# Optimization experiments

Hardware: AMD Instinct MI355X
Metric: run time of the kernel (lower is better)

The kernel has to match this reference:

```python
import jax, jax.numpy as jnp
import numpy as np

N = 50000      # nodes
D = 128        # in_dim
O = 128        # out_dim
MAX_DEG = 32   # degrees uniform in [0, MAX_DEG]


def setup_inputs() -> dict:
    rng = np.random.default_rng(0)
    deg = rng.integers(0, MAX_DEG + 1, size=N)          # includes deg==0 nodes
    dst = np.repeat(np.arange(N), deg)                  # target node per edge (grouped, like the buckets)
    E = dst.shape[0]                                    # ~800000
    src = rng.integers(0, N, size=E)                    # neighbor index per edge (flat neighbor_list)

    key = jax.random.key(0)
    k1, k2, k3, k4 = jax.random.split(key, 4)
    scale = jnp.float32(1.0 / np.sqrt(D))
    return {
        "x":  jax.random.normal(k1, (N, D), jnp.float32),
        "Wg": jax.random.normal(k2, (O, D), jnp.float32) * scale,  # global_lin.weight
        "Wl": jax.random.normal(k3, (O, D), jnp.float32) * scale,  # local_lin.weight
        "Ws": jax.random.normal(k4, (O, D), jnp.float32) * scale,  # self_lin.weight
        "b":  jnp.zeros((O,), jnp.float32),                        # bias param
        "src": jnp.asarray(src, jnp.int32),
        "dst": jnp.asarray(dst, jnp.int32),
        "deg": jnp.asarray(deg, jnp.int32),
    }


def reference(x, Wg, Wl, Ws, b, src, dst, deg):
    n = x.shape[0]
    # global branch: applied to every node
    g_out = x @ Wg.T                                           # [N, O]
    # mean-aggregate neighbor features (gather + segment-sum == the per-bucket view().mean())
    neigh_sum = jax.ops.segment_sum(x[src], dst, num_segments=n)   # [N, D]
    degf = jnp.maximum(deg, 1).astype(x.dtype)[:, None]
    neigh_mean = neigh_sum * (1.0 / degf)                       # [N, D]
    # local + self branches only for deg > 0 (deg==0 bucket keeps just global_out)
    mask = (deg > 0).astype(x.dtype)[:, None]                   # [N, 1]
    out = g_out + mask * (neigh_mean @ Wl.T + x @ Ws.T) + b
    # dropout is identity in eval mode; ELU activation
    return jax.nn.elu(out)
```

## Files before the change

### kernel.cpp

```cpp
#include <hip/hip_runtime.h>
#include <cstdint>
#include <cstddef>

#define GNPB 8
#define MNPB 16
#define GAST 264
#define DFRNG 512
#define VP_BLOCKS 16
#define VPG_BLOCKS 8

typedef __attribute__((ext_vector_type(8))) short bf16x8;
typedef __attribute__((ext_vector_type(4))) float f32x4;

static __device__ __forceinline__ unsigned short f2bf(float f) {
    unsigned int u = __builtin_bit_cast(unsigned int, f);
    u += 0x7fffu + ((u >> 16) & 1u);
    return (unsigned short)(u >> 16);
}
static __device__ __forceinline__ float bfhi(unsigned int u) { return __builtin_bit_cast(float, u & 0xFFFF0000u); }
static __device__ __forceinline__ float bflo(unsigned int u) { return __builtin_bit_cast(float, u << 16); }
static __device__ __forceinline__ void acc8(float* a, const uint4& v, unsigned m) {
    unsigned x0 = v.x & m, x1 = v.y & m, x2 = v.z & m, x3 = v.w & m;
    a[0] += bflo(x0); a[1] += bfhi(x0); a[2] += bflo(x1); a[3] += bfhi(x1);
    a[4] += bflo(x2); a[5] += bfhi(x2); a[6] += bflo(x3); a[7] += bfhi(x3);
}

__global__ __launch_bounds__(256)
void prep(const float* __restrict__ x, const float* __restrict__ Wg,
          const float* __restrict__ Wl, const float* __restrict__ Ws,
          const int* __restrict__ dst,
          unsigned short* __restrict__ Vp, unsigned short* __restrict__ Vpg,
          unsigned short* __restrict__ xb, int* __restrict__ blkoff,
          int total8, int nblk_g, int noffb, int E) {
    const int bx = blockIdx.x, t = threadIdx.x;
    if (bx < VP_BLOCKS) {
        int gid = bx * 256 + t;
        if (gid < 4096) {
            int l = gid & 63, srow = (gid >> 6) & 7, g = gid >> 9;
            int o = g * 16 + (l & 15);
            int k = srow * 32 + (l >> 4) * 8;
            uint4 u;
            if (k < 128) {
                const float* pg = Wg + o * 128 + k;
                const float* ps = Ws + o * 128 + k;
                u.x = (unsigned)f2bf(pg[0]+ps[0]) | ((unsigned)f2bf(pg[1]+ps[1]) << 16);
                u.y = (unsigned)f2bf(pg[2]+ps[2]) | ((unsigned)f2bf(pg[3]+ps[3]) << 16);
                u.z = (unsigned)f2bf(pg[4]+ps[4]) | ((unsigned)f2bf(pg[5]+ps[5]) << 16);
                u.w = (unsigned)f2bf(pg[6]+ps[6]) | ((unsigned)f2bf(pg[7]+ps[7]) << 16);
            } else {
                const float* pl = Wl + o * 128 + (k - 128);
                u.x = (unsigned)f2bf(pl[0]) | ((unsigned)f2bf(pl[1]) << 16);
                u.y = (unsigned)f2bf(pl[2]) | ((unsigned)f2bf(pl[3]) << 16);
                u.z = (unsigned)f2bf(pl[4]) | ((unsigned)f2bf(pl[5]) << 16);
                u.w = (unsigned)f2bf(pl[6]) | ((unsigned)f2bf(pl[7]) << 16);
            }
            ((uint4*)Vp)[gid] = u;
        }
    } else if (bx < VP_BLOCKS + VPG_BLOCKS) {
        int gid = (bx - VP_BLOCKS) * 256 + t;
        if (gid < 2048) {
            int l = gid & 63, s = (gid >> 6) & 3, g = gid >> 8;
            int o = g * 16 + (l & 15);
            int k = s * 32 + (l >> 4) * 8;
            const float* p = Wg + o * 128 + k;
            uint4 u;
            u.x = (unsigned)f2bf(p[0]) | ((unsigned)f2bf(p[1]) << 16);
            u.y = (unsigned)f2bf(p[2]) | ((unsigned)f2bf(p[3]) << 16);
            u.z = (unsigned)f2bf(p[4]) | ((unsigned)f2bf(p[5]) << 16);
            u.w = (unsigned)f2bf(p[6]) | ((unsigned)f2bf(p[7]) << 16);
            ((uint4*)Vpg)[gid] = u;
        }
    } else if (bx < VP_BLOCKS + VPG_BLOCKS + noffb) {
        int b = (bx - VP_BLOCKS - VPG_BLOCKS) * 256 + t;
        if (b < nblk_g) {
            int target = b * GNPB;
            int lo = 0, hi = E;
            while (lo < hi) { int mid = (lo + hi) >> 1; if (dst[mid] < target) lo = mid + 1; else hi = mid; }
            blkoff[b] = lo;
        }
    } else {
        int gid = (bx - VP_BLOCKS - VPG_BLOCKS - noffb) * 256 + t;
        if (gid < total8) {
            const float4* px = (const float4*)x + (size_t)gid * 2;
            float4 a = px[0], bq = px[1];
            uint4 u;
            u.x = (unsigned)f2bf(a.x)  | ((unsigned)f2bf(a.y)  << 16);
            u.y = (unsigned)f2bf(a.z)  | ((unsigned)f2bf(a.w)  << 16);
            u.z = (unsigned)f2bf(bq.x) | ((unsigned)f2bf(bq.y) << 16);
            u.w = (unsigned)f2bf(bq.z) | ((unsigned)f2bf(bq.w) << 16);
            ((uint4*)xb)[gid] = u;
        }
    }
}

__global__ __launch_bounds__(512, 7)
void gather(const unsigned short* __restrict__ xb, const int* __restrict__ src,
            const int* __restrict__ deg, const int* __restrict__ blkoff,
            unsigned short* __restrict__ M, int N) {
    const int t = threadIdx.x, wv = t >> 6, lane = t & 63;
    const int c = lane & 15, p = lane >> 4;
    const int base = blockIdx.x * GNPB;

    int dg8 = 0;
    if (lane < GNPB && base + lane < N) dg8 = deg[base + lane];
    int incl = dg8;
#pragma unroll
    for (int off = 1; off < GNPB; off <<= 1) {
        int v = __shfl_up(incl, off, 64);
        if (lane >= off) incl += v;
    }
    const int d = __shfl(dg8, wv, 64);
    const int s = blkoff[blockIdx.x] + __shfl(incl, wv, 64) - d;
    const int n = base + wv;
    if (n >= N) return;

    int idx = 0;
    if (lane < d) idx = src[s + lane];

    const uint4* x4 = (const uint4*)xb;
    int r0 = __shfl(idx, p, 64),      r1 = __shfl(idx, p + 4, 64);
    int r2 = __shfl(idx, p + 8, 64),  r3 = __shfl(idx, p + 12, 64);
    uint4 v0 = x4[(size_t)r0 * 16 + c], v1 = x4[(size_t)r1 * 16 + c];
    uint4 v2 = x4[(size_t)r2 * 16 + c], v3 = x4[(size_t)r3 * 16 + c];
    uint4 v4, v5, v6, v7;
    const bool two = (d > 16);
    if (two) {
        int e = 16 + p;
        int r4 = __shfl(idx, e, 64),      r5 = __shfl(idx, e + 4, 64);
        int r6 = __shfl(idx, e + 8, 64),  r7 = __shfl(idx, e + 12, 64);
        v4 = x4[(size_t)r4 * 16 + c]; v5 = x4[(size_t)r5 * 16 + c];
        v6 = x4[(size_t)r6 * 16 + c]; v7 = x4[(size_t)r7 * 16 + c];
    }
    float a[8] = {0,0,0,0,0,0,0,0};
    float b[8] = {0,0,0,0,0,0,0,0};
    acc8(a, v0, (p      < d) ? ~0u : 0u);
    acc8(b, v1, (p + 4  < d) ? ~0u : 0u);
    acc8(a, v2, (p + 8  < d) ? ~0u : 0u);
    acc8(b, v3, (p + 12 < d) ? ~0u : 0u);
    if (two) {
        int e = 16 + p;
        acc8(a, v4, (e      < d) ? ~0u : 0u);
        acc8(b, v5, (e + 4  < d) ? ~0u : 0u);
        acc8(a, v6, (e + 8  < d) ? ~0u : 0u);
        acc8(b, v7, (e + 12 < d) ? ~0u : 0u);
    }
#pragma unroll
    for (int i = 0; i < 8; ++i) a[i] += b[i];
#pragma unroll
    for (int i = 0; i < 8; ++i) {
        a[i] += __shfl_xor(a[i], 16, 64);
        a[i] += __shfl_xor(a[i], 32, 64);
    }
    if (p == 0) {
        float inv = (d > 0) ? 1.0f / (float)d : 0.0f;
        uint4 u;
        u.x = (unsigned)f2bf(a[0]*inv) | ((unsigned)f2bf(a[1]*inv) << 16);
        u.y = (unsigned)f2bf(a[2]*inv) | ((unsigned)f2bf(a[3]*inv) << 16);
        u.z = (unsigned)f2bf(a[4]*inv) | ((unsigned)f2bf(a[5]*inv) << 16);
        u.w = (unsigned)f2bf(a[6]*inv) | ((unsigned)f2bf(a[7]*inv) << 16);
        ((uint4*)M)[(size_t)n * 16 + c] = u;
    }
}

__global__ __launch_bounds__(256)
void gemm(const unsigned short* __restrict__ xb, const unsigned short* __restrict__ Mm,
          const int* __restrict__ deg, const unsigned short* __restrict__ Vp,
          const unsigned short* __restrict__ Vpg, const float* __restrict__ bias,
          float* __restrict__ out, int N, int ngemm) {
    __shared__ __align__(16) unsigned short As[MNPB * GAST];
    const int t = threadIdx.x, wv = t >> 6, lane = t & 63;
    const int c = lane & 15, quad = lane >> 4;
    const int g0 = 2 * wv, g1 = 2 * wv + 1;
    const int col0 = g0 * 16 + c, col1 = g1 * 16 + c;
    const float bv0 = bias[col0], bv1 = bias[col1];

    if (blockIdx.x >= ngemm) {
        __shared__ int nds[DFRNG];
        __shared__ int ncnt;
        const int rb = (blockIdx.x - ngemm) * DFRNG;
        if (t == 0) ncnt = 0;
        __syncthreads();
#pragma unroll
        for (int i = 0; i < DFRNG / 256; ++i) {
            int n = rb + i * 256 + t;
            if (n < N && deg[n] == 0) nds[atomicAdd(&ncnt, 1)] = n;
        }
        __syncthreads();
        const int cnt = ncnt;
        if (cnt == 0) return;
        const bf16x8* VB = (const bf16x8*)Vpg;
        for (int base = 0; base < cnt; base += 16) {
            {
                int row = t >> 4, ch = t & 15;
                int i = base + row; if (i > cnt - 1) i = cnt - 1;
                int node = nds[i];
                uint4 val = *(const uint4*)(xb + (size_t)node * 128 + ch * 8);
                *(uint4*)(As + row * GAST + ch * 8) = val;
            }
            bf16x8 b0 = VB[(g0 * 4) * 64 + lane];
            bf16x8 b1 = VB[(g1 * 4) * 64 + lane];
            __syncthreads();
            f32x4 acc0 = (f32x4){0.f,0.f,0.f,0.f};
            f32x4 acc1 = (f32x4){0.f,0.f,0.f,0.f};
#pragma unroll
            for (int s2 = 0; s2 < 4; ++s2) {
                int sn = (s2 + 1) & 3;
                bf16x8 n0 = VB[(g0 * 4 + sn) * 64 + lane];
                bf16x8 n1 = VB[(g1 * 4 + sn) * 64 + lane];
                bf16x8 a0 = *(const bf16x8*)(As + c * GAST + s2 * 32 + quad * 8);
                acc0 = __builtin_amdgcn_mfma_f32_16x16x32_bf16(a0, b0, acc0, 0, 0, 0);
                acc1 = __builtin_amdgcn_mfma_f32_16x16x32_bf16(a0, b1, acc1, 0, 0, 0);
                b0 = n0; b1 = n1;
            }
#pragma unroll
            for (int reg = 0; reg < 4; ++reg) {
                int i = base + quad * 4 + reg;
                if (i < cnt) {
                    int n = nds[i];
                    float v0 = acc0[reg] + bv0;
                    float v1 = acc1[reg] + bv1;
                    out[(size_t)n * 128 + col0] = (v0 > 0.f) ? v0 : __expf(v0) - 1.0f;
                    out[(size_t)n * 128 + col1] = (v1 > 0.f) ? v1 : __expf(v1) - 1.0f;
                }
            }
            __syncthreads();
        }
        return;
    }

    __shared__ unsigned char srowok[MNPB];
    const int base = blockIdx.x * MNPB;
    if (t < MNPB) srowok[t] = (base + t < N && deg[base + t] > 0) ? 1 : 0;
#pragma unroll
    for (int it = 0; it < 2; ++it) {
        int f = it * 256 + t;
        int row = f >> 5, ch = f & 31;
        int grow = base + row; if (grow > N - 1) grow = N - 1;
        const unsigned short* gp = (ch < 16)
            ? xb + (size_t)grow * 128 + ch * 8
            : Mm + (size_t)grow * 128 + (ch - 16) * 8;
        uint4 val = *(const uint4*)gp;
        *(uint4*)(As + row * GAST + ch * 8) = val;
    }
    const bf16x8* VB = (const bf16x8*)Vp;
    bf16x8 b0 = VB[(g0 * 8) * 64 + lane];
    bf16x8 b1 = VB[(g1 * 8) * 64 + lane];
    __syncthreads();

    f32x4 acc0 = (f32x4){0.f, 0.f, 0.f, 0.f};
    f32x4 acc1 = (f32x4){0.f, 0.f, 0.f, 0.f};
#pragma unroll
    for (int s2 = 0; s2 < 8; ++s2) {
        int sn = (s2 + 1) & 7;
        bf16x8 n0 = VB[(g0 * 8 + sn) * 64 + lane];
        bf16x8 n1 = VB[(g1 * 8 + sn) * 64 + lane];
        bf16x8 a0 = *(const bf16x8*)(As + c * GAST + s2 * 32 + quad * 8);
        acc0 = __builtin_amdgcn_mfma_f32_16x16x32_bf16(a0, b0, acc0, 0, 0, 0);
        acc1 = __builtin_amdgcn_mfma_f32_16x16x32_bf16(a0, b1, acc1, 0, 0, 0);
        b0 = n0; b1 = n1;
    }

#pragma unroll
    for (int reg = 0; reg < 4; ++reg) {
        int lrow = quad * 4 + reg;
        int grow = base + lrow;
        if (grow < N && srowok[lrow]) {
            float v0 = acc0[reg] + bv0;
            float v1 = acc1[reg] + bv1;
            out[(size_t)grow * 128 + col0] = (v0 > 0.f) ? v0 : __expf(v0) - 1.0f;
            out[(size_t)grow * 128 + col1] = (v1 > 0.f) ? v1 : __expf(v1) - 1.0f;
        }
    }
}

extern "C" void kernel_launch(void* const* d_in, const int* in_sizes, int n_in,
                              void* d_out, int out_size, void* d_ws, size_t ws_size,
                              hipStream_t stream) {
    const float* x  = (const float*)d_in[0];
    const float* Wg = (const float*)d_in[1];
    const float* Wl = (const float*)d_in[2];
    const float* Ws = (const float*)d_in[3];
    const float* b  = (const float*)d_in[4];
    const int*   src = (const int*)d_in[5];
    const int*   dst = (const int*)d_in[6];
    const int*   deg = (const int*)d_in[7];
    const int E = in_sizes[5];
    const int N = in_sizes[7];
    float* out = (float*)d_out;

    const size_t NB = (size_t)N * 128 * 2;
    unsigned short* Vp     = (unsigned short*)d_ws;
    unsigned short* Vpg    = (unsigned short*)((char*)d_ws + 65536);
    int*            blkoff = (int*)((char*)d_ws + 98304);
    unsigned short* xb     = (unsigned short*)((char*)d_ws + 131072);
    unsigned short* Mm     = (unsigned short*)((char*)d_ws + 131072 + NB);

    const int nblk_g = (N + GNPB - 1) / GNPB;
    const int noffb  = (nblk_g + 255) / 256;
    const int total8 = N * 16;
    const int nconv  = (total8 + 255) / 256;
    const int ngemm  = (N + MNPB - 1) / MNPB;
    const int ndeg   = (N + DFRNG - 1) / DFRNG;

    prep<<<dim3(VP_BLOCKS + VPG_BLOCKS + noffb + nconv), dim3(256), 0, stream>>>(
        x, Wg, Wl, Ws, dst, Vp, Vpg, xb, blkoff, total8, nblk_g, noffb, E);
    gather<<<dim3(nblk_g), dim3(512), 0, stream>>>(xb, src, deg, blkoff, Mm, N);
    gemm<<<dim3(ngemm + ndeg), dim3(256), 0, stream>>>(xb, Mm, deg, Vp, Vpg, b, out, N, ngemm);
}
```

Measured before the change: 137.9 us.

## Fuse neighbor gather-mean into the GEMM kernel via shared memory

Merges the gather kernel and the GEMM kernel into one 512-thread kernel. Each block computes the neighbor means for its 16 nodes, writes them straight into the shared A tile, then runs the MFMA GEMM. Each wave now handles one 16-column output tile instead of two. This removes the global round trip of the bf16 mean matrix and one kernel launch. In exchange it lowers the occupancy bound, and each wave does two gather passes serially before the GEMM.

```diff
diff --git a/kernel.cpp b/kernel.cpp
--- a/kernel.cpp
+++ b/kernel.cpp
@@ -93,86 +93,14 @@
     }
 }
 
-__global__ __launch_bounds__(512, 7)
-void gather(const unsigned short* __restrict__ xb, const int* __restrict__ src,
-            const int* __restrict__ deg, const int* __restrict__ blkoff,
-            unsigned short* __restrict__ M, int N) {
+__global__ __launch_bounds__(512, 5)
+void ggemm(const unsigned short* __restrict__ xb, const int* __restrict__ src,
+           const int* __restrict__ deg, const int* __restrict__ blkoff,
+           const unsigned short* __restrict__ Vp, const unsigned short* __restrict__ Vpg,
+           const float* __restrict__ bias, float* __restrict__ out, int N, int ngemm) {
+    __shared__ __align__(16) unsigned short As[MNPB * GAST];
     const int t = threadIdx.x, wv = t >> 6, lane = t & 63;
     const int c = lane & 15, p = lane >> 4;
-    const int base = blockIdx.x * GNPB;
-
-    int dg8 = 0;
-    if (lane < GNPB && base + lane < N) dg8 = deg[base + lane];
-    int incl = dg8;
-#pragma unroll
-    for (int off = 1; off < GNPB; off <<= 1) {
-        int v = __shfl_up(incl, off, 64);
-        if (lane >= off) incl += v;
-    }
-    const int d = __shfl(dg8, wv, 64);
-    const int s = blkoff[blockIdx.x] + __shfl(incl, wv, 64) - d;
-    const int n = base + wv;
-    if (n >= N) return;
-
-    int idx = 0;
-    if (lane < d) idx = src[s + lane];
-
-    const uint4* x4 = (const uint4*)xb;
-    int r0 = __shfl(idx, p, 64),      r1 = __shfl(idx, p + 4, 64);
-    int r2 = __shfl(idx, p + 8, 64),  r3 = __shfl(idx, p + 12, 64);
-    uint4 v0 = x4[(size_t)r0 * 16 + c], v1 = x4[(size_t)r1 * 16 + c];
-    uint4 v2 = x4[(size_t)r2 * 16 + c], v3 = x4[(size_t)r3 * 16 + c];
-    uint4 v4, v5, v6, v7;
-    const bool two = (d > 16);
-    if (two) {
-        int e = 16 + p;
-        int r4 = __shfl(idx, e, 64),      r5 = __shfl(idx, e + 4, 64);
-        int r6 = __shfl(idx, e + 8, 64),  r7 = __shfl(idx, e + 12, 64);
-        v4 = x4[(size_t)r4 * 16 + c]; v5 = x4[(size_t)r5 * 16 + c];
-        v6 = x4[(size_t)r6 * 16 + c]; v7 = x4[(size_t)r7 * 16 + c];
-    }
-    float a[8] = {0,0,0,0,0,0,0,0};
-    float b[8] = {0,0,0,0,0,0,0,0};
-    acc8(a, v0, (p      < d) ? ~0u : 0u);
-    acc8(b, v1, (p + 4  < d) ? ~0u : 0u);
-    acc8(a, v2, (p + 8  < d) ? ~0u : 0u);
-    acc8(b, v3, (p + 12 < d) ? ~0u : 0u);
-    if (two) {
-        int e = 16 + p;
-        acc8(a, v4, (e      < d) ? ~0u : 0u);
-        acc8(b, v5, (e + 4  < d) ? ~0u : 0u);
-        acc8(a, v6, (e + 8  < d) ? ~0u : 0u);
-        acc8(b, v7, (e + 12 < d) ? ~0u : 0u);
-    }
-#pragma unroll
-    for (int i = 0; i < 8; ++i) a[i] += b[i];
-#pragma unroll
-    for (int i = 0; i < 8; ++i) {
-        a[i] += __shfl_xor(a[i], 16, 64);
-        a[i] += __shfl_xor(a[i], 32, 64);
-    }
-    if (p == 0) {
-        float inv = (d > 0) ? 1.0f / (float)d : 0.0f;
-        uint4 u;
-        u.x = (unsigned)f2bf(a[0]*inv) | ((unsigned)f2bf(a[1]*inv) << 16);
-        u.y = (unsigned)f2bf(a[2]*inv) | ((unsigned)f2bf(a[3]*inv) << 16);
-        u.z = (unsigned)f2bf(a[4]*inv) | ((unsigned)f2bf(a[5]*inv) << 16);
-        u.w = (unsigned)f2bf(a[6]*inv) | ((unsigned)f2bf(a[7]*inv) << 16);
-        ((uint4*)M)[(size_t)n * 16 + c] = u;
-    }
-}
-
-__global__ __launch_bounds__(256)
-void gemm(const unsigned short* __restrict__ xb, const unsigned short* __restrict__ Mm,
-          const int* __restrict__ deg, const unsigned short* __restrict__ Vp,
-          const unsigned short* __restrict__ Vpg, const float* __restrict__ bias,
-          float* __restrict__ out, int N, int ngemm) {
-    __shared__ __align__(16) unsigned short As[MNPB * GAST];
-    const int t = threadIdx.x, wv = t >> 6, lane = t & 63;
-    const int c = lane & 15, quad = lane >> 4;
-    const int g0 = 2 * wv, g1 = 2 * wv + 1;
-    const int col0 = g0 * 16 + c, col1 = g1 * 16 + c;
-    const float bv0 = bias[col0], bv1 = bias[col1];
 
     if (blockIdx.x >= ngemm) {
         __shared__ int nds[DFRNG];
@@ -180,47 +108,42 @@
         const int rb = (blockIdx.x - ngemm) * DFRNG;
         if (t == 0) ncnt = 0;
         __syncthreads();
-#pragma unroll
-        for (int i = 0; i < DFRNG / 256; ++i) {
-            int n = rb + i * 256 + t;
+        {
+            int n = rb + t;
             if (n < N && deg[n] == 0) nds[atomicAdd(&ncnt, 1)] = n;
         }
         __syncthreads();
         const int cnt = ncnt;
         if (cnt == 0) return;
         const bf16x8* VB = (const bf16x8*)Vpg;
+        const int col = wv * 16 + c;
+        const float bv = bias[col];
         for (int base = 0; base < cnt; base += 16) {
-            {
+            if (t < 256) {
                 int row = t >> 4, ch = t & 15;
                 int i = base + row; if (i > cnt - 1) i = cnt - 1;
                 int node = nds[i];
-                uint4 val = *(const uint4*)(xb + (size_t)node * 128 + ch * 8);
-                *(uint4*)(As + row * GAST + ch * 8) = val;
-            }
-            bf16x8 b0 = VB[(g0 * 4) * 64 + lane];
-            bf16x8 b1 = VB[(g1 * 4) * 64 + lane];
+                *(uint4*)(As + row * GAST + ch * 8) =
+                    *(const uint4*)(xb + (size_t)node * 128 + ch * 8);
+            }
+            bf16x8 b0 = VB[(wv * 4) * 64 + lane];
             __syncthreads();
-            f32x4 acc0 = (f32x4){0.f,0.f,0.f,0.f};
-            f32x4 acc1 = (f32x4){0.f,0.f,0.f,0.f};
+            f32x4 acc = (f32x4){0.f, 0.f, 0.f, 0.f};
 #pragma unroll
             for (int s2 = 0; s2 < 4; ++s2) {
                 int sn = (s2 + 1) & 3;
-                bf16x8 n0 = VB[(g0 * 4 + sn) * 64 + lane];
-                bf16x8 n1 = VB[(g1 * 4 + sn) * 64 + lane];
-                bf16x8 a0 = *(const bf16x8*)(As + c * GAST + s2 * 32 + quad * 8);
-                acc0 = __builtin_amdgcn_mfma_f32_16x16x32_bf16(a0, b0, acc0, 0, 0, 0);
-                acc1 = __builtin_amdgcn_mfma_f32_16x16x32_bf16(a0, b1, acc1, 0, 0, 0);
-                b0 = n0; b1 = n1;
+                bf16x8 n0 = VB[(wv * 4 + sn) * 64 + lane];
+                bf16x8 a0 = *(const bf16x8*)(As + c * GAST + s2 * 32 + p * 8);
+                acc = __builtin_amdgcn_mfma_f32_16x16x32_bf16(a0, b0, acc, 0, 0, 0);
+                b0 = n0;
             }
 #pragma unroll
             for (int reg = 0; reg < 4; ++reg) {
-                int i = base + quad * 4 + reg;
+                int i = base + p * 4 + reg;
                 if (i < cnt) {
                     int n = nds[i];
-                    float v0 = acc0[reg] + bv0;
-                    float v1 = acc1[reg] + bv1;
-                    out[(size_t)n * 128 + col0] = (v0 > 0.f) ? v0 : __expf(v0) - 1.0f;
-                    out[(size_t)n * 128 + col1] = (v1 > 0.f) ? v1 : __expf(v1) - 1.0f;
+                    float v = acc[reg] + bv;
+                    out[(size_t)n * 128 + col] = (v > 0.f) ? v : __expf(v) - 1.0f;
                 }
             }
             __syncthreads();
@@ -228,47 +151,103 @@
         return;
     }
 
-    __shared__ unsigned char srowok[MNPB];
     const int base = blockIdx.x * MNPB;
-    if (t < MNPB) srowok[t] = (base + t < N && deg[base + t] > 0) ? 1 : 0;
-#pragma unroll
-    for (int it = 0; it < 2; ++it) {
-        int f = it * 256 + t;
-        int row = f >> 5, ch = f & 31;
+    if (t < 256) {
+        int row = t >> 4, ch = t & 15;
         int grow = base + row; if (grow > N - 1) grow = N - 1;
-        const unsigned short* gp = (ch < 16)
-            ? xb + (size_t)grow * 128 + ch * 8
-            : Mm + (size_t)grow * 128 + (ch - 16) * 8;
-        uint4 val = *(const uint4*)gp;
-        *(uint4*)(As + row * GAST + ch * 8) = val;
-    }
+        *(uint4*)(As + row * GAST + ch * 8) =
+            *(const uint4*)(xb + (size_t)grow * 128 + ch * 8);
+    }
+
+    int dg16 = 0;
+    if (lane < 16 && base + lane < N) dg16 = deg[base + lane];
+    int incl = dg16;
+#pragma unroll
+    for (int off = 1; off < 16; off <<= 1) {
+        int v = __shfl_up(incl, off, 64);
+        if (lane >= off) incl += v;
+    }
+    const int blk_s = blkoff[blockIdx.x * 2];
+    const uint4* x4 = (const uint4*)xb;
+
+#pragma unroll 1
+    for (int half = 0; half < 2; ++half) {
+        const int j = wv + half * 8;
+        const int d = __shfl(dg16, j, 64);
+        const int s = blk_s + __shfl(incl, j, 64) - d;
+        const bool valid = (base + j < N);
+
+        int idx = 0;
+        if (valid && lane < d) idx = src[s + lane];
+
+        int r0 = __shfl(idx, p, 64),      r1 = __shfl(idx, p + 4, 64);
+        int r2 = __shfl(idx, p + 8, 64),  r3 = __shfl(idx, p + 12, 64);
+        uint4 v0 = x4[(size_t)r0 * 16 + c], v1 = x4[(size_t)r1 * 16 + c];
+        uint4 v2 = x4[(size_t)r2 * 16 + c], v3 = x4[(size_t)r3 * 16 + c];
+        uint4 v4, v5, v6, v7;
+        const bool two = (d > 16);
+        if (two) {
+            int e = 16 + p;
+            int r4 = __shfl(idx, e, 64),      r5 = __shfl(idx, e + 4, 64);
+            int r6 = __shfl(idx, e + 8, 64),  r7 = __shfl(idx, e + 12, 64);
+            v4 = x4[(size_t)r4 * 16 + c]; v5 = x4[(size_t)r5 * 16 + c];
+            v6 = x4[(size_t)r6 * 16 + c]; v7 = x4[(size_t)r7 * 16 + c];
+        }
+        float a[8] = {0,0,0,0,0,0,0,0};
+        float b[8] = {0,0,0,0,0,0,0,0};
+        acc8(a, v0, (p      < d) ? ~0u : 0u);
+        acc8(b, v1, (p + 4  < d) ? ~0u : 0u);
+        acc8(a, v2, (p + 8  < d) ? ~0u : 0u);
+        acc8(b, v3, (p + 12 < d) ? ~0u : 0u);
+        if (two) {
+            int e = 16 + p;
+            acc8(a, v4, (e      < d) ? ~0u : 0u);
+            acc8(b, v5, (e + 4  < d) ? ~0u : 0u);
+            acc8(a, v6, (e + 8  < d) ? ~0u : 0u);
+            acc8(b, v7, (e + 12 < d) ? ~0u : 0u);
+        }
+#pragma unroll
+        for (int i = 0; i < 8; ++i) a[i] += b[i];
+#pragma unroll
+        for (int i = 0; i < 8; ++i) {
+            a[i] += __shfl_xor(a[i], 16, 64);
+            a[i] += __shfl_xor(a[i], 32, 64);
+        }
+        if (p == 0 && valid) {
+            float inv = (d > 0) ? 1.0f / (float)d : 0.0f;
+            uint4 u;
+            u.x = (unsigned)f2bf(a[0]*inv) | ((unsigned)f2bf(a[1]*inv) << 16);
+            u.y = (unsigned)f2bf(a[2]*inv) | ((unsigned)f2bf(a[3]*inv) << 16);
+            u.z = (unsigned)f2bf(a[4]*inv) | ((unsigned)f2bf(a[5]*inv) << 16);
+            u.w = (unsigned)f2bf(a[6]*inv) | ((unsigned)f2bf(a[7]*inv) << 16);
+            *(uint4*)(As + j * GAST + 128 + c * 8) = u;
+        }
+    }
+
     const bf16x8* VB = (const bf16x8*)Vp;
-    bf16x8 b0 = VB[(g0 * 8) * 64 + lane];
-    bf16x8 b1 = VB[(g1 * 8) * 64 + lane];
+    bf16x8 b0 = VB[(wv * 8) * 64 + lane];
     __syncthreads();
 
-    f32x4 acc0 = (f32x4){0.f, 0.f, 0.f, 0.f};
-    f32x4 acc1 = (f32x4){0.f, 0.f, 0.f, 0.f};
+    f32x4 acc = (f32x4){0.f, 0.f, 0.f, 0.f};
 #pragma unroll
     for (int s2 = 0; s2 < 8; ++s2) {
         int sn = (s2 + 1) & 7;
-        bf16x8 n0 = VB[(g0 * 8 + sn) * 64 + lane];
-        bf16x8 n1 = VB[(g1 * 8 + sn) * 64 + lane];
-        bf16x8 a0 = *(const bf16x8*)(As + c * GAST + s2 * 32 + quad * 8);
-        acc0 = __builtin_amdgcn_mfma_f32_16x16x32_bf16(a0, b0, acc0, 0, 0, 0);
-        acc1 = __builtin_amdgcn_mfma_f32_16x16x32_bf16(a0, b1, acc1, 0, 0, 0);
-        b0 = n0; b1 = n1;
-    }
-
+        bf16x8 n0 = VB[(wv * 8 + sn) * 64 + lane];
+        bf16x8 a0 = *(const bf16x8*)(As + c * GAST + s2 * 32 + p * 8);
+        acc = __builtin_amdgcn_mfma_f32_16x16x32_bf16(a0, b0, acc, 0, 0, 0);
+        b0 = n0;
+    }
+
+    const int col = wv * 16 + c;
+    const float bv = bias[col];
 #pragma unroll
     for (int reg = 0; reg < 4; ++reg) {
-        int lrow = quad * 4 + reg;
+        int lrow = p * 4 + reg;
         int grow = base + lrow;
-        if (grow < N && srowok[lrow]) {
-            float v0 = acc0[reg] + bv0;
-            float v1 = acc1[reg] + bv1;
-            out[(size_t)grow * 128 + col0] = (v0 > 0.f) ? v0 : __expf(v0) - 1.0f;
-            out[(size_t)grow * 128 + col1] = (v1 > 0.f) ? v1 : __expf(v1) - 1.0f;
+        int rdeg = __shfl(dg16, lrow, 64);
+        if (grow < N && rdeg > 0) {
+            float v = acc[reg] + bv;
+            out[(size_t)grow * 128 + col] = (v > 0.f) ? v : __expf(v) - 1.0f;
         }
     }
 }
@@ -288,12 +267,10 @@
     const int N = in_sizes[7];
     float* out = (float*)d_out;
 
-    const size_t NB = (size_t)N * 128 * 2;
     unsigned short* Vp     = (unsigned short*)d_ws;
     unsigned short* Vpg    = (unsigned short*)((char*)d_ws + 65536);
     int*            blkoff = (int*)((char*)d_ws + 98304);
     unsigned short* xb     = (unsigned short*)((char*)d_ws + 131072);
-    unsigned short* Mm     = (unsigned short*)((char*)d_ws + 131072 + NB);
 
     const int nblk_g = (N + GNPB - 1) / GNPB;
     const int noffb  = (nblk_g + 255) / 256;
@@ -304,6 +281,6 @@
 
     prep<<<dim3(VP_BLOCKS + VPG_BLOCKS + noffb + nconv), dim3(256), 0, stream>>>(
         x, Wg, Wl, Ws, dst, Vp, Vpg, xb, blkoff, total8, nblk_g, noffb, E);
-    gather<<<dim3(nblk_g), dim3(512), 0, stream>>>(xb, src, deg, blkoff, Mm, N);
-    gemm<<<dim3(ngemm + ndeg), dim3(256), 0, stream>>>(xb, Mm, deg, Vp, Vpg, b, out, N, ngemm);
-}
+    ggemm<<<dim3(ngemm + ndeg), dim3(512), 0, stream>>>(
+        xb, src, deg, blkoff, Vp, Vpg, b, out, N, ngemm);
+}
```

Measured after the change: 139.7 us. No clear change (+1.3%).
